# Kernel optimization log

Measured on AMD Instinct MI355X. Metric: run time of the kernel, lower is better.

Reference implementation:

```python
import jax, jax.numpy as jnp
import numpy as np

H = 256; DS = 8; DC = 4; DI = 512; DTR = 16; NH = 4; EPS = 1e-5
B, N, F, E, S, LC = 8, 512, 32, 8192, 512, 8


def setup_inputs() -> dict:
    key = jax.random.key(0)
    ks = iter(jax.random.split(key, 64))
    def rn(shape, s=0.05):
        return jax.random.normal(next(ks), shape, jnp.float32) * s
    z = lambda *s: jnp.zeros(s, jnp.float32)
    inp = dict(
        node_features=jax.random.normal(next(ks), (B, N, F), jnp.float32),
        edge_index=jax.random.randint(next(ks), (B, 2, E), 0, N),
        W_init=rn((F, H)), b_init=z(H),
        gcn1_W=rn((H, H)), gcn1_b=z(H),
        gcn2_W=rn((H, H)), gcn2_b=z(H),
        in_proj_W=rn((H, 2 * DI)),
        conv_W=rn((DI, DC)), conv_b=z(DI),
        xproj_W=rn((DI, DTR + 2 * DS)),
        dt_W=rn((DTR, DI)), dt_b=z(DI),
        A_log=jnp.log(jnp.tile(jnp.arange(1, DS + 1, dtype=jnp.float32), (DI, 1))),
        Dp=jnp.ones((DI,), jnp.float32),
        out_W=rn((DI, H)),
        Wq=rn((H, H)), bq=z(H), Wk=rn((H, H)), bk=z(H), Wv=rn((H, H)), bv=z(H),
        Wo=rn((H, H)), bo=z(H),
        fus_W=rn((3 * H, H)), fus_b=z(H),
        ln_g=jnp.ones((H,), jnp.float32), ln_b=z(H),
        cw=rn((H, 1)), cb=z(1), hw=rn((H, 4)), hb=z(4), tw=rn((H, 3)), tb=z(3),
        p1w=rn((H, S)), p1b=z(S), p2w=rn((H, S)), p2b=z(S),
        dw=rn((H, S)), db=z(S), sw=rn((H, LC)), sb=z(LC))
    return inp


def gcn(x, src, dst, W, b):
    # PyG GCNConv: self-loops + symmetric deg^{-1/2} normalization, scatter-add.
    n = x.shape[0]
    loops = jnp.arange(n)
    s = jnp.concatenate([src, loops]); d = jnp.concatenate([dst, loops])
    deg = jax.ops.segment_sum(jnp.ones_like(d, x.dtype), d, n)
    dinv = jnp.where(deg > 0, jax.lax.rsqrt(deg), 0.0)
    norm = (dinv[s] * dinv[d])[:, None]
    m = x @ W
    return jax.ops.segment_sum(m[s] * norm, d, n) + b


def mamba(x, in_W, conv_W, conv_b, xproj_W, dt_W, dt_b, A_log, Dp, out_W):
    # mamba_ssm Mamba block, batch=1, seq len L = total nodes.
    L = x.shape[0]
    xz = x @ in_W
    xc, zg = xz[:, :DI], xz[:, DI:]
    xp = jnp.pad(xc, ((DC - 1, 0), (0, 0)))            # causal depthwise conv
    win = xp[jnp.arange(L)[:, None] + jnp.arange(DC)[None, :]]  # [L,K,DI]
    xc = jax.nn.silu(jnp.einsum('lkd,dk->ld', win, conv_W) + conv_b)
    proj = xc @ xproj_W
    dt, Bm, Cm = proj[:, :DTR], proj[:, DTR:DTR + DS], proj[:, DTR + DS:]
    delta = jax.nn.softplus(dt @ dt_W + dt_b)           # [L,DI]
    A = -jnp.exp(A_log)                                 # [DI,DS]
    dA = jnp.exp(delta[:, :, None] * A[None])           # [L,DI,DS]
    dBx = delta[:, :, None] * Bm[:, None, :] * xc[:, :, None]
    def step(h, inp):
        dA_t, dBx_t, C_t = inp
        h = dA_t * h + dBx_t
        return h, (h * C_t[None, :]).sum(-1)
    _, y = jax.lax.scan(step, jnp.zeros((DI, DS), x.dtype), (dA, dBx, Cm))
    y = (y + Dp * xc) * jax.nn.silu(zg)
    return y @ out_W


def mha(x, Wq, bq, Wk, bk, Wv, bv, Wo, bo):
    L = x.shape[0]; hd = H // NH
    q = (x @ Wq + bq).reshape(L, NH, hd)
    k = (x @ Wk + bk).reshape(L, NH, hd)
    v = (x @ Wv + bv).reshape(L, NH, hd)
    s = jnp.einsum('qhd,khd->hqk', q, k) / np.float32(np.sqrt(hd))
    a = jax.nn.softmax(s, axis=-1)
    o = jnp.einsum('hqk,khd->qhd', a, v).reshape(L, H)
    return o @ Wo + bo


def _forward(node_features, edge_index, W_init, b_init, gcn1_W, gcn1_b, gcn2_W, gcn2_b,
             in_proj_W, conv_W, conv_b, xproj_W, dt_W, dt_b, A_log, Dp, out_W,
             Wq, bq, Wk, bk, Wv, bv, Wo, bo, fus_W, fus_b, ln_g, ln_b,
             cw, cb, hw, hb, tw, tb, p1w, p1b, p2w, p2b, dw, db, sw, sb):
    Bsz, Nn, Ff = node_features.shape
    x = node_features.reshape(Bsz * Nn, Ff)
    # offset per-graph edge indices into the flat node space (batching loop)
    ei = (edge_index + (jnp.arange(Bsz) * Nn)[:, None, None]).transpose(1, 0, 2).reshape(2, -1)
    src, dst = ei[0], ei[1]
    h = jax.nn.relu(x @ W_init + b_init)
    h = jax.nn.relu(gcn(h, src, dst, gcn1_W, gcn1_b))
    h = jax.nn.relu(gcn(h, src, dst, gcn2_W, gcn2_b))
    m = mamba(h, in_proj_W, conv_W, conv_b, xproj_W, dt_W, dt_b, A_log, Dp, out_W)
    a = mha(h, Wq, bq, Wk, bk, Wv, bv, Wo, bo)
    fused = jax.nn.relu(jnp.concatenate([h, m, a], -1) @ fus_W + fus_b)
    res = fused + h
    mu = res.mean(-1, keepdims=True)
    var = ((res - mu) ** 2).mean(-1, keepdims=True)
    hf = (res - mu) * jax.lax.rsqrt(var + EPS) * ln_g + ln_b
    batch = jnp.repeat(jnp.arange(Bsz), Nn)
    pooled = jax.ops.segment_sum(hf, batch, Bsz) / jnp.float32(Nn)  # global_mean_pool
    outs = [pooled @ cw + cb, pooled @ hw + hb, pooled @ tw + tb,
            pooled @ p1w + p1b, pooled @ p2w + p2b, pooled @ dw + db,
            pooled @ sw + sb]
    return jnp.concatenate(outs, -1)  # [B, 1+4+3+S+S+S+LC]


def reference(node_features, edge_index, W_init, b_init, gcn1_W, gcn1_b, gcn2_W, gcn2_b,
              in_proj_W, conv_W, conv_b, xproj_W, dt_W, dt_b, A_log, Dp, out_W,
              Wq, bq, Wk, bk, Wv, bv, Wo, bo, fus_W, fus_b, ln_g, ln_b,
              cw, cb, hw, hb, tw, tb, p1w, p1b, p2w, p2b, dw, db, sw, sb):
    return _forward(node_features, edge_index, W_init, b_init, gcn1_W, gcn1_b, gcn2_W, gcn2_b,
                    in_proj_W, conv_W, conv_b, xproj_W, dt_W, dt_b, A_log, Dp, out_W,
                    Wq, bq, Wk, bk, Wv, bv, Wo, bo, fus_W, fus_b, ln_g, ln_b,
                    cw, cb, hw, hb, tw, tb, p1w, p1b, p2w, p2b, dw, db, sw, sb)
```

## Files before the change

kernel.cpp:

```cpp
#include <hip/hip_runtime.h>
#include <hip/hip_bf16.h>
#include <math.h>

typedef __hip_bfloat16 hbf;
typedef short bf16x8 __attribute__((ext_vector_type(8)));
typedef float f32x4 __attribute__((ext_vector_type(4)));

constexpr int NL  = 4096;
constexpr int HH  = 256;
constexpr int NE  = 8192;
constexpr int DIc = 512;
constexpr int DSc = 8;
constexpr int CLc = 16;
constexpr int NOUT = 12416;

constexpr size_t O_MBUF  = 0;
constexpr size_t O_QK    = 1048576;
constexpr size_t O_H2    = 2097152;
constexpr size_t O_CATB  = 3145728;
constexpr size_t O_XZB   = 4718592;
constexpr size_t O_XC    = 6815744;
constexpr size_t O_DELTA = 8912896;
constexpr size_t O_PROJ  = 11010048;
constexpr size_t O_HST   = 11141120;
constexpr size_t O_Y     = 12189696;
constexpr size_t O_POOL  = 13238272;
constexpr size_t O_DINV  = 13240320;
constexpr size_t O_B768  = 13244416;
constexpr size_t O_INT   = 13245184;
constexpr size_t O_WT    = 13327112;
constexpr size_t O_XB    = 13839112;
constexpr size_t O_H0B   = 13904648;
constexpr size_t O_H2B   = 14428936;
constexpr size_t O_XCB   = 14953224;
constexpr size_t O_DTAB  = 16001800;
constexpr size_t O_QKB   = 16067584;
constexpr size_t O_VTB   = 17116160;
constexpr size_t O_PART  = 17640448;
constexpr size_t O_HWT   = 17902592;

constexpr int NW = 12;
__device__ __constant__ int wc_cum[NW+1] = {
    0, 8192, 73728, 139264, 155648, 172032, 303104, 565248,
    630784, 696320, 761856, 827392, 1024000 };
__device__ __constant__ int wc_K [NW] = {32,256,256,512,16,512,256,256,256,256,256,768};
__device__ __constant__ int wc_N [NW] = {256,256,256,32,512,256,1024,256,256,256,256,256};
__device__ __constant__ int wc_Kp[NW] = {32,256,256,512,32,512,256,256,256,256,256,768};
struct WSrc { const float* p[NW]; };
struct HSrc { const float* p[7]; };
struct OPtrs { hbf* p[8]; };

__device__ __constant__ int hw_b[8]  = {0,1,5,8,520,1032,1544,1552};
__device__ __constant__ int hw_nc[7] = {1,4,3,512,512,512,8};

constexpr int PR_W = 1024000;
constexpr int PR_X = PR_W + 131072;
constexpr int PR_B = PR_X + 768;
constexpr int PR_P = PR_B + 262144;
constexpr int PR_I = PR_P + 4096;
constexpr int PR_H = PR_I + 397312;
__global__ __launch_bounds__(256) void prep_k(WSrc ws, hbf* __restrict__ wt,
        const float* __restrict__ x, hbf* __restrict__ xb,
        const float* __restrict__ bq, const float* __restrict__ bk,
        const float* __restrict__ bv,
        float* __restrict__ b768, float* __restrict__ part, int* __restrict__ indeg,
        HSrc hs, float* __restrict__ hwt) {
    int idx = blockIdx.x*256 + threadIdx.x;
    if (idx < PR_W) {
        int lo = 0, hi = NW-1;
        while (lo < hi) { int mid = (lo+hi+1)>>1; if (idx >= wc_cum[mid]) lo = mid; else hi = mid-1; }
        int local = idx - wc_cum[lo];
        int Kp = wc_Kp[lo], K = wc_K[lo], N = wc_N[lo];
        int n = local / Kp, k = local - n*Kp;
        float v = (k < K) ? ws.p[lo][(size_t)k*N + n] : 0.0f;
        wt[idx] = __float2bfloat16(v);
    } else if (idx < PR_X) {
        int i = idx - PR_W;
        xb[i] = __float2bfloat16(x[i]);
    } else if (idx < PR_B) {
        int i = idx - PR_X;
        b768[i] = (i < 256) ? bq[i] : (i < 512 ? bk[i-256] : bv[i-512]);
    } else if (idx < PR_P) {
        part[idx - PR_B] = 0.0f;
    } else if (idx < PR_I) {
        indeg[idx - PR_P] = 0;
    } else if (idx < PR_H) {
        int i = idx - PR_I;
        int j = i >> 8, k = i & 255;
        int seg = 0;
        while (j >= hw_b[seg+1]) seg++;
        int col = j - hw_b[seg], nc = hw_nc[seg];
        hwt[(size_t)j*256 + k] = hs.p[seg][(size_t)k*nc + col];
    }
}

__global__ void count_k(const int* __restrict__ ei, int* __restrict__ indeg) {
    int i = blockIdx.x*256 + threadIdx.x;
    int b = i >> 13, e = i & 8191;
    int dst = ei[b*2*NE + NE + e] + (b << 9);
    atomicAdd(&indeg[dst], 1);
}

__global__ __launch_bounds__(1024) void prefix_k(const int* __restrict__ indeg,
                                                 int* __restrict__ row_start,
                                                 int* __restrict__ cursor,
                                                 float* __restrict__ dinv) {
    __shared__ int part[1024];
    int t = threadIdx.x;
    int v0[4]; int s = 0;
    #pragma unroll
    for (int i = 0; i < 4; i++) {
        int cnt = indeg[t*4 + i];
        v0[i] = s; s += cnt;
        dinv[t*4 + i] = rsqrtf(1.0f + (float)cnt);
    }
    part[t] = s;
    __syncthreads();
    for (int o = 1; o < 1024; o <<= 1) {
        int x = (t >= o) ? part[t-o] : 0;
        __syncthreads();
        part[t] += x;
        __syncthreads();
    }
    int base = (t > 0) ? part[t-1] : 0;
    #pragma unroll
    for (int i = 0; i < 4; i++) {
        int rs = base + v0[i];
        row_start[t*4+i] = rs; cursor[t*4+i] = rs;
    }
    if (t == 1023) row_start[4096] = part[1023];
}

__global__ void scatter_k(const int* __restrict__ ei, int* __restrict__ cursor,
                          int* __restrict__ csr) {
    int i = blockIdx.x*256 + threadIdx.x;
    int b = i >> 13, e = i & 8191;
    int src = ei[b*2*NE + e]       + (b << 9);
    int dst = ei[b*2*NE + NE + e]  + (b << 9);
    int pos = atomicAdd(&cursor[dst], 1);
    csr[pos] = src;
}

template<int MODE>
__global__ __launch_bounds__(256) void gather_k(const float* __restrict__ m,
                        const int* __restrict__ csr, const int* __restrict__ row_start,
                        const float* __restrict__ dinv, const float* __restrict__ bias,
                        float* __restrict__ out, hbf* __restrict__ outb,
                        hbf* __restrict__ catb) {
    int n = blockIdx.x, c = threadIdx.x;
    float dn = dinv[n];
    float acc = m[(size_t)n*HH + c] * dn * dn;
    int e0 = row_start[n], e1 = row_start[n+1];
    for (int e = e0; e < e1; e++) {
        int s = csr[e];
        acc += m[(size_t)s*HH + c] * (dinv[s] * dn);
    }
    float r = fmaxf(acc + bias[c], 0.0f);
    if (MODE) {
        out[(size_t)n*HH + c] = r;
        catb[(size_t)n*768 + c] = __float2bfloat16(r);
    }
    outb[(size_t)n*HH + c] = __float2bfloat16(r);
}

template<int ACT, int OUTM>
__global__ __launch_bounds__(512) void mg_k(const unsigned short* __restrict__ A,
        const unsigned short* __restrict__ Bt, const float* __restrict__ bias,
        void* __restrict__ Cp, int ldc, void* __restrict__ Cp2, void* __restrict__ Cp3,
        const float* __restrict__ resid, int ldr, int M, int K, int N)
{
    __shared__ __align__(16) unsigned short Asm[2][64][40];
    __shared__ __align__(16) unsigned short Bsm[2][64][40];
    int t = threadIdx.x;
    int lane = t & 63, w = t >> 6;
    int wm = w & 3, wn = w >> 2;
    int row0 = blockIdx.x * 64, col0 = blockIdx.y * 64;
    int sr = t >> 3;
    int sk8 = (t & 7) * 8;
    int su = sk8 >> 5, so = sk8 & 31;
    f32x4 acc0 = {}, acc1 = {};
    int fr = lane & 15, fq8 = (lane >> 4) * 8;

    uint4 zz = make_uint4(0u,0u,0u,0u);
    uint4 ra = zz, rb = zz;
    bool bnv = (col0 + sr) < N;
    if (sk8 < K) {
        ra = *(const uint4*)&A[(size_t)(row0+sr)*K + sk8];
        if (bnv) rb = *(const uint4*)&Bt[(size_t)(col0+sr)*K + sk8];
    }

    for (int k0 = 0; k0 < K; k0 += 64) {
        __syncthreads();
        *(uint4*)&Asm[su][sr][so] = ra;
        *(uint4*)&Bsm[su][sr][so] = rb;
        __syncthreads();
        int kn = k0 + 64;
        if (kn < K) {
            ra = rb = zz;
            if (kn + sk8 < K) {
                ra = *(const uint4*)&A[(size_t)(row0+sr)*K + kn + sk8];
                if (bnv) rb = *(const uint4*)&Bt[(size_t)(col0+sr)*K + kn + sk8];
            }
        }
        #pragma unroll
        for (int ks = 0; ks < 2; ks++) {
            bf16x8 a  = *(bf16x8*)&Asm[ks][wm*16 + fr][fq8];
            bf16x8 b0 = *(bf16x8*)&Bsm[ks][wn*32 + fr][fq8];
            bf16x8 b1 = *(bf16x8*)&Bsm[ks][wn*32 + 16 + fr][fq8];
            acc0 = __builtin_amdgcn_mfma_f32_16x16x32_bf16(a, b0, acc0, 0, 0, 0);
            acc1 = __builtin_amdgcn_mfma_f32_16x16x32_bf16(a, b1, acc1, 0, 0, 0);
        }
    }

    int fc = lane & 15, frq = (lane >> 4) * 4;
    if constexpr (OUTM == 4) {
        #pragma unroll
        for (int nt = 0; nt < 2; nt++) {
            int col = col0 + wn*32 + nt*16 + fc;
            if (col >= 32) continue;
            f32x4& av = nt ? acc1 : acc0;
            #pragma unroll
            for (int i = 0; i < 4; i++) {
                int row = row0 + wm*16 + frq + i;
                float v = av[i];
                ((float*)Cp)[(size_t)row*32 + col] = v;
                ((hbf*)Cp2)[(size_t)row*32 + col] = __float2bfloat16((col < 16) ? v : 0.0f);
            }
        }
    } else if constexpr (OUTM == 5) {
        if (col0 < 1024) {
            #pragma unroll
            for (int nt = 0; nt < 2; nt++) {
                int col = col0 + wn*32 + nt*16 + fc;
                f32x4& av = nt ? acc1 : acc0;
                #pragma unroll
                for (int i = 0; i < 4; i++) {
                    int row = row0 + wm*16 + frq + i;
                    ((hbf*)Cp)[(size_t)row*1024 + col] = __float2bfloat16(av[i]);
                }
            }
        } else if (col0 < 1536) {
            #pragma unroll
            for (int nt = 0; nt < 2; nt++) {
                int gcol = col0 + wn*32 + nt*16 + fc;
                int col = gcol - 1024;
                float bvv = bias[col];
                float sc = (col < 256) ? 0.125f : 1.0f;
                f32x4& av = nt ? acc1 : acc0;
                #pragma unroll
                for (int i = 0; i < 4; i++) {
                    int row = row0 + wm*16 + frq + i;
                    ((hbf*)Cp2)[(size_t)row*512 + col] = __float2bfloat16((av[i] + bvv) * sc);
                }
            }
        } else {
            __shared__ __align__(16) unsigned short Ts[64][72];
            #pragma unroll
            for (int nt = 0; nt < 2; nt++) {
                int gcol = col0 + wn*32 + nt*16 + fc;
                float bvv = bias[gcol - 1024];
                f32x4& av = nt ? acc1 : acc0;
                #pragma unroll
                for (int i = 0; i < 4; i++)
                    *(hbf*)&Ts[wn*32 + nt*16 + fc][wm*16 + frq + i] = __float2bfloat16(av[i] + bvv);
            }
            __syncthreads();
            int c = t >> 3, rs = (t & 7) * 8;
            *(uint4*)((hbf*)Cp3 + (size_t)(col0 - 1536 + c)*NL + row0 + rs) = *(uint4*)&Ts[c][rs];
        }
    } else {
        #pragma unroll
        for (int nt = 0; nt < 2; nt++) {
            int col = col0 + wn*32 + nt*16 + fc;
            if (col >= N) continue;
            float bvv = bias ? bias[col] : 0.0f;
            f32x4& av = nt ? acc1 : acc0;
            #pragma unroll
            for (int i = 0; i < 4; i++) {
                int row = row0 + wm*16 + frq + i;
                float v = av[i] + bvv;
                if (ACT == 1) v = fmaxf(v, 0.0f);
                if (ACT == 2) v = (v > 20.0f) ? v : log1pf(expf(v));
                if (resid) v += resid[(size_t)row*ldr + col];
                if (OUTM == 0) ((float*)Cp)[(size_t)row*ldc + col] = v;
                else           ((hbf*)Cp)[(size_t)row*ldc + col] = __float2bfloat16(v);
            }
        }
    }
}

__global__ void conv_k(const hbf* __restrict__ xzb, const float* __restrict__ cW,
                       const float* __restrict__ cb, hbf* __restrict__ xcb) {
    int i = blockIdx.x*256 + threadIdx.x;
    int l = i >> 9, d = i & 511;
    float acc = cb[d];
    #pragma unroll
    for (int k = 0; k < 4; k++) {
        int ls = l - 3 + k;
        if (ls >= 0) acc += __bfloat162float(xzb[(size_t)ls*1024 + d]) * cW[d*4 + k];
    }
    float r = acc / (1.0f + __expf(-acc));
    xcb[i] = __float2bfloat16(r);
}

__global__ __launch_bounds__(256) void scan1_k(const float* __restrict__ delta,
                        const hbf* __restrict__ xc, const float* __restrict__ proj,
                        const float* __restrict__ Alog,
                        float* __restrict__ P, float* __restrict__ Hl)
{
    int c = blockIdx.x >> 1;
    int d = ((blockIdx.x & 1) << 8) + threadIdx.x;
    float Ac[DSc], pr[DSc], h[DSc];
    #pragma unroll
    for (int s2 = 0; s2 < DSc; s2++) { Ac[s2] = -__expf(Alog[d*DSc+s2]); pr[s2]=1.0f; h[s2]=0.0f; }
    int l0 = c * CLc;
    for (int l = l0; l < l0 + CLc; l++) {
        float dl = delta[(size_t)l*DIc + d];
        float dx = dl * __bfloat162float(xc[(size_t)l*DIc + d]);
        const float* pb = proj + l*32 + 16;
        #pragma unroll
        for (int s2 = 0; s2 < DSc; s2++) {
            float a = __expf(dl * Ac[s2]);
            h[s2] = a*h[s2] + dx*pb[s2];
            pr[s2] *= a;
        }
    }
    #pragma unroll
    for (int s2 = 0; s2 < DSc; s2++) {
        P [(size_t)(c*DSc+s2)*DIc + d] = pr[s2];
        Hl[(size_t)(c*DSc+s2)*DIc + d] = h[s2];
    }
}

__global__ __launch_bounds__(256) void scan2t_k(const float* __restrict__ P,
                        const float* __restrict__ Hl, float* __restrict__ Hst) {
    __shared__ float Ps[256][17], Hs[256][17];
    int t = threadIdx.x, sg = blockIdx.x;
    int si = t & 15, cb = t >> 4;
    #pragma unroll
    for (int it = 0; it < 16; it++) {
        int c = it*16 + cb;
        size_t off = (size_t)c*4096 + sg*16 + si;
        Ps[c][si] = P[off];
        Hs[c][si] = Hl[off];
    }
    __syncthreads();
    int si2 = t >> 4, g = t & 15;
    int lane = t & 63;
    float Pg = 1.0f, Hg = 0.0f;
    #pragma unroll
    for (int j = 0; j < 16; j++) {
        int c = g*16 + j;
        float pc = Ps[c][si2], hc = Hs[c][si2];
        Hg = hc + pc*Hg;
        Pg = pc*Pg;
    }
    #pragma unroll
    for (int off = 1; off < 16; off <<= 1) {
        float Pp = __shfl(Pg, lane - off);
        float Hp = __shfl(Hg, lane - off);
        if (g >= off) { Hg = Hg + Pg*Hp; Pg = Pg*Pp; }
    }
    float carry = __shfl(Hg, lane - 1);
    if (g == 0) carry = 0.0f;
    float h = carry;
    #pragma unroll
    for (int j = 0; j < 16; j++) {
        int c = g*16 + j;
        float pc = Ps[c][si2], hc = Hs[c][si2];
        Hs[c][si2] = h;
        h = hc + pc*h;
    }
    __syncthreads();
    #pragma unroll
    for (int it = 0; it < 16; it++) {
        int c = it*16 + cb;
        Hst[(size_t)c*4096 + sg*16 + si] = Hs[c][si];
    }
}

__global__ __launch_bounds__(256) void scan3_k(const float* __restrict__ delta,
                        const hbf* __restrict__ xc, const float* __restrict__ proj,
                        const float* __restrict__ Alog, const float* __restrict__ Hst,
                        const float* __restrict__ Dp, const hbf* __restrict__ xzb,
                        hbf* __restrict__ Y)
{
    int c = blockIdx.x >> 1;
    int d = ((blockIdx.x & 1) << 8) + threadIdx.x;
    float Ac[DSc], h[DSc];
    #pragma unroll
    for (int s2 = 0; s2 < DSc; s2++) {
        Ac[s2] = -__expf(Alog[d*DSc+s2]);
        h[s2]  = Hst[(size_t)(c*DSc+s2)*DIc + d];
    }
    float dpv = Dp[d];
    int l0 = c * CLc;
    for (int l = l0; l < l0 + CLc; l++) {
        float dl = delta[(size_t)l*DIc + d];
        float xv = __bfloat162float(xc[(size_t)l*DIc + d]);
        float dx = dl * xv;
        const float* pb = proj + l*32 + 16;
        float y = 0.0f;
        #pragma unroll
        for (int s2 = 0; s2 < DSc; s2++) {
            float a = __expf(dl * Ac[s2]);
            h[s2] = a*h[s2] + dx*pb[s2];
            y += h[s2] * pb[8+s2];
        }
        float z = __bfloat162float(xzb[(size_t)l*1024 + 512 + d]);
        float sz = z / (1.0f + __expf(-z));
        Y[(size_t)l*DIc + d] = __float2bfloat16((y + dpv*xv) * sz);
    }
}

__global__ __launch_bounds__(512, 8) void attn_part_k(const unsigned short* __restrict__ QK,
                       const unsigned short* __restrict__ Vt,
                       OPtrs op, float* __restrict__ lsum)
{
    __shared__ __align__(16) unsigned short QPs[128][72];
    __shared__ __align__(16) unsigned short Ks[64][72];
    __shared__ __align__(16) unsigned short Vs[64][72];
    int t = threadIdx.x, lane = t & 63, w = t >> 6;
    int h = blockIdx.y, q0 = blockIdx.x * 128, skc = blockIdx.z;
    int fm = lane & 15, fq = lane >> 4;

    {
        int qr = t >> 2, qc = (t & 3) * 16;
        const unsigned short* src = &QK[(size_t)(q0+qr)*512 + h*64 + qc];
        *(uint4*)&QPs[qr][qc]     = *(const uint4*)&src[0];
        *(uint4*)&QPs[qr][qc + 8] = *(const uint4*)&src[8];
    }
    __syncthreads();
    bf16x8 qa[2];
    #pragma unroll
    for (int ks = 0; ks < 2; ks++)
        qa[ks] = *(bf16x8*)&QPs[w*16 + fm][ks*32 + fq*8];

    bf16x8 ones;
    #pragma unroll
    for (int j = 0; j < 8; j++) ones[j] = (short)0x3F80;

    f32x4 o[4] = {};
    f32x4 ol = {};
    int sr = t >> 3, sk = (t & 7) * 8;
    const unsigned short* Kb = QK + 256;
    int kt = skc * 512;
    uint4 ka = *(const uint4*)&Kb[(size_t)(kt+sr)*512 + h*64 + sk];
    uint4 va = *(const uint4*)&Vt[(size_t)(h*64+sr)*NL + kt + sk];

    for (int it = 0; it < 8; it++) {
        __syncthreads();
        *(uint4*)&Ks[sr][sk] = ka;
        *(uint4*)&Vs[sr][sk] = va;
        __syncthreads();
        if (it < 7) {
            int kn = kt + 64;
            ka = *(const uint4*)&Kb[(size_t)(kn+sr)*512 + h*64 + sk];
            va = *(const uint4*)&Vt[(size_t)(h*64+sr)*NL + kn + sk];
        }
        f32x4 s[4] = {};
        #pragma unroll
        for (int ks = 0; ks < 2; ks++) {
            #pragma unroll
            for (int nt = 0; nt < 4; nt++) {
                bf16x8 kb = *(bf16x8*)&Ks[nt*16 + fm][ks*32 + fq*8];
                s[nt] = __builtin_amdgcn_mfma_f32_16x16x32_bf16(qa[ks], kb, s[nt], 0, 0, 0);
            }
        }
        #pragma unroll
        for (int nt = 0; nt < 4; nt++)
            #pragma unroll
            for (int i = 0; i < 4; i++) {
                float p = __expf(s[nt][i] - 4.0f);
                *(hbf*)&QPs[w*16 + fq*4 + i][nt*16 + fm] = __float2bfloat16(p);
            }
        #pragma unroll
        for (int ks = 0; ks < 2; ks++) {
            bf16x8 pa = *(bf16x8*)&QPs[w*16 + fm][ks*32 + fq*8];
            #pragma unroll
            for (int nt = 0; nt < 4; nt++) {
                bf16x8 vb = *(bf16x8*)&Vs[nt*16 + fm][ks*32 + fq*8];
                o[nt] = __builtin_amdgcn_mfma_f32_16x16x32_bf16(pa, vb, o[nt], 0, 0, 0);
            }
            ol = __builtin_amdgcn_mfma_f32_16x16x32_bf16(pa, ones, ol, 0, 0, 0);
        }
        kt += 64;
    }
    hbf* Op = op.p[skc];
    #pragma unroll
    for (int i = 0; i < 4; i++) {
        int row = w*16 + fq*4 + i;
        #pragma unroll
        for (int nt = 0; nt < 4; nt++)
            Op[(size_t)(q0 + row)*HH + h*64 + nt*16 + fm] = __float2bfloat16(o[nt][i]);
    }
    if (fm == 0) {
        #pragma unroll
        for (int i = 0; i < 4; i++)
            lsum[(size_t)(skc*4 + h)*NL + q0 + w*16 + fq*4 + i] = ol[i];
    }
}

__global__ __launch_bounds__(256) void amerge_k(OPtrs op, const float* __restrict__ lsum,
                                                hbf* __restrict__ aob) {
    int row = blockIdx.x, t = threadIdx.x, h = t >> 6;
    float L = 0.0f, s = 0.0f;
    #pragma unroll
    for (int c = 0; c < 8; c++) {
        L += lsum[(size_t)(c*4 + h)*NL + row];
        s += __bfloat162float(op.p[c][(size_t)row*HH + t]);
    }
    aob[(size_t)row*HH + t] = __float2bfloat16(s / L);
}

__global__ __launch_bounds__(256) void ln_k(const float* __restrict__ X,
                    const float* __restrict__ g, const float* __restrict__ b,
                    float* __restrict__ part) {
    __shared__ float red[4];
    int r = blockIdx.x, t = threadIdx.x;
    float v = X[(size_t)r*HH + t];
    float s = v;
    #pragma unroll
    for (int o = 32; o > 0; o >>= 1) s += __shfl_down(s, o);
    if ((t & 63) == 0) red[t >> 6] = s;
    __syncthreads();
    float mean = (red[0]+red[1]+red[2]+red[3]) * (1.0f/256.0f);
    float dfv = v - mean;
    float s2 = dfv*dfv;
    #pragma unroll
    for (int o = 32; o > 0; o >>= 1) s2 += __shfl_down(s2, o);
    __syncthreads();
    if ((t & 63) == 0) red[t >> 6] = s2;
    __syncthreads();
    float var = (red[0]+red[1]+red[2]+red[3]) * (1.0f/256.0f);
    float y = dfv * rsqrtf(var + 1e-5f) * g[t] + b[t];
    atomicAdd(&part[(size_t)(r & 127)*2048 + (r >> 9)*HH + t], y * (1.0f/512.0f));
}

__global__ void reduce_k(const float* __restrict__ part, float* __restrict__ pooled) {
    int i = blockIdx.x*256 + threadIdx.x;
    float s = 0.0f;
    #pragma unroll 8
    for (int p = 0; p < 128; p++) s += part[(size_t)p*2048 + i];
    pooled[i] = s;
}

__global__ __launch_bounds__(256) void heads_k(const float* __restrict__ pooled,
        const float* __restrict__ hwt,
        const float* cbh, const float* hb, const float* tb, const float* p1b,
        const float* p2b, const float* db, const float* sb, float* __restrict__ out)
{
    int idx = blockIdx.x*4 + (threadIdx.x >> 6);
    int lane = threadIdx.x & 63;
    if (idx >= NOUT) return;
    int b = idx / 1552, j = idx - b*1552;
    const float* bi; int col;
    if (j < 1)         { bi = cbh; col = j;        }
    else if (j < 5)    { bi = hb;  col = j - 1;    }
    else if (j < 8)    { bi = tb;  col = j - 5;    }
    else if (j < 520)  { bi = p1b; col = j - 8;    }
    else if (j < 1032) { bi = p2b; col = j - 520;  }
    else if (j < 1544) { bi = db;  col = j - 1032; }
    else               { bi = sb;  col = j - 1544; }
    const float* pl = pooled + b*HH;
    const float* wr = hwt + (size_t)j*256;
    float s = 0.0f;
    #pragma unroll
    for (int k = lane; k < 256; k += 64) s = fmaf(pl[k], wr[k], s);
    #pragma unroll
    for (int o = 32; o > 0; o >>= 1) s += __shfl_down(s, o);
    if (lane == 0) out[idx] = s + bi[col];
}

extern "C" void kernel_launch(void* const* d_in, const int* in_sizes, int n_in,
                              void* d_out, int out_size, void* d_ws, size_t ws_size,
                              hipStream_t stream)
{
    (void)in_sizes; (void)n_in; (void)out_size; (void)ws_size;
    const float* x      = (const float*)d_in[0];
    const int*   ei     = (const int*)  d_in[1];
    const float* W_init = (const float*)d_in[2];
    const float* b_init = (const float*)d_in[3];
    const float* g1W = (const float*)d_in[4];
    const float* g1b = (const float*)d_in[5];
    const float* g2W = (const float*)d_in[6];
    const float* g2b = (const float*)d_in[7];
    const float* inW = (const float*)d_in[8];
    const float* cW  = (const float*)d_in[9];
    const float* cb  = (const float*)d_in[10];
    const float* xpW = (const float*)d_in[11];
    const float* dtW = (const float*)d_in[12];
    const float* dtb = (const float*)d_in[13];
    const float* Alog= (const float*)d_in[14];
    const float* Dp  = (const float*)d_in[15];
    const float* outW= (const float*)d_in[16];
    const float* Wq  = (const float*)d_in[17];
    const float* bq  = (const float*)d_in[18];
    const float* Wk  = (const float*)d_in[19];
    const float* bk  = (const float*)d_in[20];
    const float* Wv  = (const float*)d_in[21];
    const float* bv  = (const float*)d_in[22];
    const float* Wo  = (const float*)d_in[23];
    const float* bo  = (const float*)d_in[24];
    const float* fusW= (const float*)d_in[25];
    const float* fusb= (const float*)d_in[26];
    const float* lng = (const float*)d_in[27];
    const float* lnb = (const float*)d_in[28];
    const float* cwp = (const float*)d_in[29];
    const float* cbp = (const float*)d_in[30];
    const float* hwp = (const float*)d_in[31];
    const float* hbp = (const float*)d_in[32];
    const float* twp = (const float*)d_in[33];
    const float* tbp = (const float*)d_in[34];
    const float* p1w = (const float*)d_in[35];
    const float* p1b = (const float*)d_in[36];
    const float* p2w = (const float*)d_in[37];
    const float* p2b = (const float*)d_in[38];
    const float* dwp = (const float*)d_in[39];
    const float* dbp = (const float*)d_in[40];
    const float* swp = (const float*)d_in[41];
    const float* sbp = (const float*)d_in[42];

    float* fw = (float*)d_ws;
    int* iw = (int*)(fw + O_INT);
    int* indeg = iw;
    int* row_start = iw + 4096;
    int* cursor = iw + 8193;
    int* csr = iw + 12289;
    float* dinv = fw + O_DINV;

    hbf* wt   = (hbf*)(fw + O_WT);
    hbf* xb   = (hbf*)(fw + O_XB);
    hbf* h0b  = (hbf*)(fw + O_H0B);
    hbf* h2b  = (hbf*)(fw + O_H2B);
    hbf* xcb  = (hbf*)(fw + O_XCB);
    hbf* dtab = (hbf*)(fw + O_DTAB);
    hbf* xzb  = (hbf*)(fw + O_XZB);
    hbf* yb   = (hbf*)(fw + O_Y);
    hbf* aob  = (hbf*)(fw + O_Y);
    hbf* catb = (hbf*)(fw + O_CATB);
    hbf* qkB  = (hbf*)(fw + O_QKB);
    hbf* vtB  = (hbf*)(fw + O_VTB);
    float* fused = fw + O_XC;
    float* b768 = fw + O_B768;
    float* part = fw + O_PART;
    float* hwt  = fw + O_HWT;

    float* scanP  = fw + O_MBUF;
    float* scanHl = fw + O_QK;
    float* scanHst= fw + O_HST;
    float* lsum   = fw + O_HST;

    OPtrs op;
    op.p[0] = (hbf*)(fw + O_MBUF);
    op.p[1] = (hbf*)(fw + O_MBUF + 524288);
    op.p[2] = (hbf*)(fw + O_DELTA);
    op.p[3] = (hbf*)(fw + O_DELTA + 524288);
    op.p[4] = (hbf*)(fw + O_DELTA + 1048576);
    op.p[5] = (hbf*)(fw + O_DELTA + 1572864);
    op.p[6] = (hbf*)(fw + O_XZB);
    op.p[7] = (hbf*)(fw + O_XZB + 524288);

    hbf* WtInit  = wt + 0;
    hbf* WtG1    = wt + 8192;
    hbf* WtG2    = wt + 73728;
    hbf* WtXp    = wt + 139264;
    hbf* WtDt    = wt + 155648;
    hbf* WtOut   = wt + 172032;
    hbf* WtInQKV = wt + 303104;
    hbf* WtO     = wt + 761856;
    hbf* WtFus   = wt + 827392;

    WSrc wsrc;
    wsrc.p[0]=W_init; wsrc.p[1]=g1W; wsrc.p[2]=g2W; wsrc.p[3]=xpW; wsrc.p[4]=dtW;
    wsrc.p[5]=outW; wsrc.p[6]=inW; wsrc.p[7]=Wq; wsrc.p[8]=Wk; wsrc.p[9]=Wv;
    wsrc.p[10]=Wo; wsrc.p[11]=fusW;
    HSrc hsrc;
    hsrc.p[0]=cwp; hsrc.p[1]=hwp; hsrc.p[2]=twp; hsrc.p[3]=p1w;
    hsrc.p[4]=p2w; hsrc.p[5]=dwp; hsrc.p[6]=swp;
    prep_k<<<(PR_H+255)/256,256,0,stream>>>(wsrc, wt, x, xb, bq, bk, bv, b768,
                                            part, indeg, hsrc, hwt);

    count_k<<<256,256,0,stream>>>(ei, indeg);
    prefix_k<<<1,1024,0,stream>>>(indeg, row_start, cursor, dinv);
    scatter_k<<<256,256,0,stream>>>(ei, cursor, csr);

    mg_k<1,1><<<dim3(64,4),512,0,stream>>>((const unsigned short*)xb, (const unsigned short*)WtInit,
        b_init, h0b, 256, nullptr, nullptr, nullptr, 0, NL, 32, 256);
    mg_k<0,0><<<dim3(64,4),512,0,stream>>>((const unsigned short*)h0b, (const unsigned short*)WtG1,
        nullptr, fw+O_MBUF, 256, nullptr, nullptr, nullptr, 0, NL, 256, 256);
    gather_k<0><<<4096,256,0,stream>>>(fw+O_MBUF, csr, row_start, dinv, g1b, nullptr, h0b, nullptr);
    mg_k<0,0><<<dim3(64,4),512,0,stream>>>((const unsigned short*)h0b, (const unsigned short*)WtG2,
        nullptr, fw+O_MBUF, 256, nullptr, nullptr, nullptr, 0, NL, 256, 256);
    gather_k<1><<<4096,256,0,stream>>>(fw+O_MBUF, csr, row_start, dinv, g2b, fw+O_H2, h2b, catb);

    mg_k<0,5><<<dim3(64,28),512,0,stream>>>((const unsigned short*)h2b, (const unsigned short*)WtInQKV,
        b768, xzb, 1024, qkB, vtB, nullptr, 0, NL, 256, 1792);

    conv_k<<<8192,256,0,stream>>>(xzb, cW, cb, xcb);
    mg_k<0,4><<<dim3(64,1),512,0,stream>>>((const unsigned short*)xcb, (const unsigned short*)WtXp,
        nullptr, fw+O_PROJ, 32, dtab, nullptr, nullptr, 0, NL, 512, 32);
    mg_k<2,0><<<dim3(64,8),512,0,stream>>>((const unsigned short*)dtab, (const unsigned short*)WtDt,
        dtb, fw+O_DELTA, 512, nullptr, nullptr, nullptr, 0, NL, 32, 512);
    scan1_k<<<512,256,0,stream>>>(fw+O_DELTA, xcb, fw+O_PROJ, Alog, scanP, scanHl);
    scan2t_k<<<256,256,0,stream>>>(scanP, scanHl, scanHst);
    scan3_k<<<512,256,0,stream>>>(fw+O_DELTA, xcb, fw+O_PROJ, Alog, scanHst, Dp, xzb, yb);
    mg_k<0,1><<<dim3(64,4),512,0,stream>>>((const unsigned short*)yb, (const unsigned short*)WtOut,
        nullptr, catb + 256, 768, nullptr, nullptr, nullptr, 0, NL, 512, 256);

    attn_part_k<<<dim3(32,4,8),512,0,stream>>>((const unsigned short*)qkB,
        (const unsigned short*)vtB, op, lsum);
    amerge_k<<<4096,256,0,stream>>>(op, lsum, aob);
    mg_k<0,1><<<dim3(64,4),512,0,stream>>>((const unsigned short*)aob, (const unsigned short*)WtO,
        bo, catb + 512, 768, nullptr, nullptr, nullptr, 0, NL, 256, 256);

    mg_k<1,0><<<dim3(64,4),512,0,stream>>>((const unsigned short*)catb, (const unsigned short*)WtFus,
        fusb, fused, 256, nullptr, nullptr, fw+O_H2, 256, NL, 768, 256);
    ln_k<<<4096,256,0,stream>>>(fused, lng, lnb, part);
    reduce_k<<<8,256,0,stream>>>(part, fw+O_POOL);
    heads_k<<<(NOUT+3)/4,256,0,stream>>>(fw+O_POOL, hwt, cbp,hbp,tbp,p1b,p2b,dbp,sbp,
                                         (float*)d_out);
}
```

Measured before the change: 353.8 us.

## Fuse attention merge into Wo GEMM and LayerNorm into fusion GEMM

Adds a wide-tile GEMM kernel (16 rows by 256 cols per block) with two variants. The first folds the split-K attention merge into the A-operand load of the Wo projection. The second applies bias, ReLU, the residual and LayerNorm, then pools with atomics, all in the fusion GEMM epilogue. This drops the amerge_k and ln_k launches and the intermediate aob and fused buffers. The attention score loop is also restructured to compute two tiles at a time, which lowers register pressure. In exchange, LayerNorm variance is now computed as E[x^2]-mu^2, and each block runs only 256 blocks with 16-row tiles.

```diff
diff --git a/kernel.cpp b/kernel.cpp
--- a/kernel.cpp
+++ b/kernel.cpp
@@ -289,6 +289,149 @@
     }
 }
 
+__device__ __forceinline__ uint4 merge_load(const OPtrs& op, const float* __restrict__ lsum,
+                                            int row, int d0) {
+    int head = d0 >> 6;
+    float L = 0.0f;
+    #pragma unroll
+    for (int c = 0; c < 8; c++) L += lsum[(size_t)(c*4 + head)*NL + row];
+    float inv = 1.0f / L;
+    float sums[8] = {};
+    #pragma unroll
+    for (int c = 0; c < 8; c++) {
+        uint4 ov = *(const uint4*)&((const unsigned short*)op.p[c])[(size_t)row*HH + d0];
+        const hbf* oh = (const hbf*)&ov;
+        #pragma unroll
+        for (int j = 0; j < 8; j++) sums[j] += __bfloat162float(oh[j]);
+    }
+    uint4 av;
+    hbf* ah = (hbf*)&av;
+    #pragma unroll
+    for (int j = 0; j < 8; j++) ah[j] = __float2bfloat16(sums[j] * inv);
+    return av;
+}
+
+template<int W>
+__global__ __launch_bounds__(512) void mgw_k(const unsigned short* __restrict__ A,
+        const unsigned short* __restrict__ Bt, const float* __restrict__ bias,
+        hbf* __restrict__ Cb, OPtrs op, const float* __restrict__ lsum,
+        const float* __restrict__ resid, const float* __restrict__ g,
+        const float* __restrict__ bb, float* __restrict__ part, int K)
+{
+    constexpr int KT = (W == 0) ? 4 : 12;
+    __shared__ __align__(16) unsigned short As[2][16][40];
+    __shared__ __align__(16) unsigned short Bs[2][256][40];
+    __shared__ float redS[16][8], redQ[16][8], mval[16], rstd[16];
+    int t = threadIdx.x, lane = t & 63, w = t >> 6;
+    int row0 = blockIdx.x * 16;
+    int fr = lane & 15, fq8 = (lane >> 4) * 8;
+    int sr = t >> 3, sk8 = (t & 7) * 8;
+    f32x4 acc0 = {}, acc1 = {};
+
+    uint4 rb[4]; uint4 ra;
+    #pragma unroll
+    for (int ii = 0; ii < 4; ii++) {
+        int idx = t + ii*512;
+        rb[ii] = *(const uint4*)&Bt[(size_t)(idx >> 3)*K + ((idx & 7) * 8)];
+    }
+    if (t < 128) {
+        if constexpr (W == 0) ra = merge_load(op, lsum, row0 + sr, sk8);
+        else                  ra = *(const uint4*)&A[(size_t)(row0 + sr)*768 + sk8];
+    }
+
+    for (int kt = 0; kt < KT; kt++) {
+        __syncthreads();
+        #pragma unroll
+        for (int ii = 0; ii < 4; ii++) {
+            int idx = t + ii*512;
+            int k8 = (idx & 7) * 8;
+            *(uint4*)&Bs[k8 >> 5][idx >> 3][k8 & 31] = rb[ii];
+        }
+        if (t < 128) *(uint4*)&As[sk8 >> 5][sr][sk8 & 31] = ra;
+        __syncthreads();
+        if (kt + 1 < KT) {
+            int kn = (kt + 1) * 64;
+            #pragma unroll
+            for (int ii = 0; ii < 4; ii++) {
+                int idx = t + ii*512;
+                rb[ii] = *(const uint4*)&Bt[(size_t)(idx >> 3)*K + kn + ((idx & 7) * 8)];
+            }
+            if (t < 128) {
+                if constexpr (W == 0) ra = merge_load(op, lsum, row0 + sr, kn + sk8);
+                else                  ra = *(const uint4*)&A[(size_t)(row0 + sr)*768 + kn + sk8];
+            }
+        }
+        #pragma unroll
+        for (int ks = 0; ks < 2; ks++) {
+            bf16x8 a  = *(bf16x8*)&As[ks][fr][fq8];
+            bf16x8 b0 = *(bf16x8*)&Bs[ks][w*32 + fr][fq8];
+            bf16x8 b1 = *(bf16x8*)&Bs[ks][w*32 + 16 + fr][fq8];
+            acc0 = __builtin_amdgcn_mfma_f32_16x16x32_bf16(a, b0, acc0, 0, 0, 0);
+            acc1 = __builtin_amdgcn_mfma_f32_16x16x32_bf16(a, b1, acc1, 0, 0, 0);
+        }
+    }
+
+    int fc = lane & 15, frq = (lane >> 4) * 4;
+    if constexpr (W == 0) {
+        #pragma unroll
+        for (int nt = 0; nt < 2; nt++) {
+            int col = w*32 + nt*16 + fc;
+            float bvv = bias[col];
+            f32x4& av = nt ? acc1 : acc0;
+            #pragma unroll
+            for (int i = 0; i < 4; i++) {
+                int row = row0 + frq + i;
+                Cb[(size_t)row*768 + col] = __float2bfloat16(av[i] + bvv);
+            }
+        }
+    } else {
+        float v[2][4];
+        #pragma unroll
+        for (int nt = 0; nt < 2; nt++) {
+            int col = w*32 + nt*16 + fc;
+            float bvv = bias[col];
+            f32x4& av = nt ? acc1 : acc0;
+            #pragma unroll
+            for (int i = 0; i < 4; i++) {
+                int row = row0 + frq + i;
+                v[nt][i] = fmaxf(av[i] + bvv, 0.0f) + resid[(size_t)row*HH + col];
+            }
+        }
+        #pragma unroll
+        for (int i = 0; i < 4; i++) {
+            float s = v[0][i] + v[1][i];
+            float q = v[0][i]*v[0][i] + v[1][i]*v[1][i];
+            #pragma unroll
+            for (int o = 1; o < 16; o <<= 1) {
+                s += __shfl_xor(s, o);
+                q += __shfl_xor(q, o);
+            }
+            if (fc == 0) { redS[frq + i][w] = s; redQ[frq + i][w] = q; }
+        }
+        __syncthreads();
+        if (t < 16) {
+            float s = 0.0f, q = 0.0f;
+            #pragma unroll
+            for (int j = 0; j < 8; j++) { s += redS[t][j]; q += redQ[t][j]; }
+            float mu = s * (1.0f/256.0f);
+            float var = q * (1.0f/256.0f) - mu*mu;
+            mval[t] = mu; rstd[t] = rsqrtf(var + 1e-5f);
+        }
+        __syncthreads();
+        #pragma unroll
+        for (int nt = 0; nt < 2; nt++) {
+            int col = w*32 + nt*16 + fc;
+            float gv = g[col], bv2 = bb[col];
+            #pragma unroll
+            for (int i = 0; i < 4; i++) {
+                int r = frq + i, row = row0 + r;
+                float y = (v[nt][i] - mval[r]) * rstd[r] * gv + bv2;
+                atomicAdd(&part[(size_t)(row & 127)*2048 + (row >> 9)*HH + col], y * (1.0f/512.0f));
+            }
+        }
+    }
+}
+
 __global__ void conv_k(const hbf* __restrict__ xzb, const float* __restrict__ cW,
                        const float* __restrict__ cb, hbf* __restrict__ xcb) {
     int i = blockIdx.x*256 + threadIdx.x;
@@ -458,22 +601,24 @@
             ka = *(const uint4*)&Kb[(size_t)(kn+sr)*512 + h*64 + sk];
             va = *(const uint4*)&Vt[(size_t)(h*64+sr)*NL + kn + sk];
         }
-        f32x4 s[4] = {};
-        #pragma unroll
-        for (int ks = 0; ks < 2; ks++) {
-            #pragma unroll
-            for (int nt = 0; nt < 4; nt++) {
-                bf16x8 kb = *(bf16x8*)&Ks[nt*16 + fm][ks*32 + fq*8];
-                s[nt] = __builtin_amdgcn_mfma_f32_16x16x32_bf16(qa[ks], kb, s[nt], 0, 0, 0);
-            }
-        }
-        #pragma unroll
-        for (int nt = 0; nt < 4; nt++)
+        #pragma unroll
+        for (int np = 0; np < 2; np++) {
+            f32x4 s0 = {}, s1 = {};
+            #pragma unroll
+            for (int ks = 0; ks < 2; ks++) {
+                bf16x8 kb0 = *(bf16x8*)&Ks[(np*2+0)*16 + fm][ks*32 + fq*8];
+                bf16x8 kb1 = *(bf16x8*)&Ks[(np*2+1)*16 + fm][ks*32 + fq*8];
+                s0 = __builtin_amdgcn_mfma_f32_16x16x32_bf16(qa[ks], kb0, s0, 0, 0, 0);
+                s1 = __builtin_amdgcn_mfma_f32_16x16x32_bf16(qa[ks], kb1, s1, 0, 0, 0);
+            }
             #pragma unroll
             for (int i = 0; i < 4; i++) {
-                float p = __expf(s[nt][i] - 4.0f);
-                *(hbf*)&QPs[w*16 + fq*4 + i][nt*16 + fm] = __float2bfloat16(p);
-            }
+                float p0 = __expf(s0[i] - 4.0f);
+                float p1 = __expf(s1[i] - 4.0f);
+                *(hbf*)&QPs[w*16 + fq*4 + i][(np*2+0)*16 + fm] = __float2bfloat16(p0);
+                *(hbf*)&QPs[w*16 + fq*4 + i][(np*2+1)*16 + fm] = __float2bfloat16(p1);
+            }
+        }
         #pragma unroll
         for (int ks = 0; ks < 2; ks++) {
             bf16x8 pa = *(bf16x8*)&QPs[w*16 + fm][ks*32 + fq*8];
@@ -499,42 +644,6 @@
         for (int i = 0; i < 4; i++)
             lsum[(size_t)(skc*4 + h)*NL + q0 + w*16 + fq*4 + i] = ol[i];
     }
-}
-
-__global__ __launch_bounds__(256) void amerge_k(OPtrs op, const float* __restrict__ lsum,
-                                                hbf* __restrict__ aob) {
-    int row = blockIdx.x, t = threadIdx.x, h = t >> 6;
-    float L = 0.0f, s = 0.0f;
-    #pragma unroll
-    for (int c = 0; c < 8; c++) {
-        L += lsum[(size_t)(c*4 + h)*NL + row];
-        s += __bfloat162float(op.p[c][(size_t)row*HH + t]);
-    }
-    aob[(size_t)row*HH + t] = __float2bfloat16(s / L);
-}
-
-__global__ __launch_bounds__(256) void ln_k(const float* __restrict__ X,
-                    const float* __restrict__ g, const float* __restrict__ b,
-                    float* __restrict__ part) {
-    __shared__ float red[4];
-    int r = blockIdx.x, t = threadIdx.x;
-    float v = X[(size_t)r*HH + t];
-    float s = v;
-    #pragma unroll
-    for (int o = 32; o > 0; o >>= 1) s += __shfl_down(s, o);
-    if ((t & 63) == 0) red[t >> 6] = s;
-    __syncthreads();
-    float mean = (red[0]+red[1]+red[2]+red[3]) * (1.0f/256.0f);
-    float dfv = v - mean;
-    float s2 = dfv*dfv;
-    #pragma unroll
-    for (int o = 32; o > 0; o >>= 1) s2 += __shfl_down(s2, o);
-    __syncthreads();
-    if ((t & 63) == 0) red[t >> 6] = s2;
-    __syncthreads();
-    float var = (red[0]+red[1]+red[2]+red[3]) * (1.0f/256.0f);
-    float y = dfv * rsqrtf(var + 1e-5f) * g[t] + b[t];
-    atomicAdd(&part[(size_t)(r & 127)*2048 + (r >> 9)*HH + t], y * (1.0f/512.0f));
 }
 
 __global__ void reduce_k(const float* __restrict__ part, float* __restrict__ pooled) {
@@ -637,11 +746,9 @@
     hbf* dtab = (hbf*)(fw + O_DTAB);
     hbf* xzb  = (hbf*)(fw + O_XZB);
     hbf* yb   = (hbf*)(fw + O_Y);
-    hbf* aob  = (hbf*)(fw + O_Y);
     hbf* catb = (hbf*)(fw + O_CATB);
     hbf* qkB  = (hbf*)(fw + O_QKB);
     hbf* vtB  = (hbf*)(fw + O_VTB);
-    float* fused = fw + O_XC;
     float* b768 = fw + O_B768;
     float* part = fw + O_PART;
     float* hwt  = fw + O_HWT;
@@ -710,13 +817,12 @@
 
     attn_part_k<<<dim3(32,4,8),512,0,stream>>>((const unsigned short*)qkB,
         (const unsigned short*)vtB, op, lsum);
-    amerge_k<<<4096,256,0,stream>>>(op, lsum, aob);
-    mg_k<0,1><<<dim3(64,4),512,0,stream>>>((const unsigned short*)aob, (const unsigned short*)WtO,
-        bo, catb + 512, 768, nullptr, nullptr, nullptr, 0, NL, 256, 256);
-
-    mg_k<1,0><<<dim3(64,4),512,0,stream>>>((const unsigned short*)catb, (const unsigned short*)WtFus,
-        fusb, fused, 256, nullptr, nullptr, fw+O_H2, 256, NL, 768, 256);
-    ln_k<<<4096,256,0,stream>>>(fused, lng, lnb, part);
+    mgw_k<0><<<256,512,0,stream>>>(nullptr, (const unsigned short*)WtO, bo,
+        catb + 512, op, lsum, nullptr, nullptr, nullptr, nullptr, 256);
+
+    mgw_k<1><<<256,512,0,stream>>>((const unsigned short*)catb, (const unsigned short*)WtFus,
+        fusb, nullptr, op, nullptr, fw+O_H2, lng, lnb, part, 768);
+
     reduce_k<<<8,256,0,stream>>>(part, fw+O_POOL);
     heads_k<<<(NOUT+3)/4,256,0,stream>>>(fw+O_POOL, hwt, cbp,hbp,tbp,p1b,p2b,dbp,sbp,
                                          (float*)d_out);
```

Measured after the change: 376.8 us. 6.5% more time.

## Aggregate before transform in GCN layers and add MFMA priority hints in attention

Applied to the files above, without the earlier changes.

GCN layers now reorder A·(X·W) into (A·X)·W. The neighbour gather reads bf16 activations instead of fp32 matmul outputs, and bias plus ReLU move into the GEMM epilogue. A new OUTM=6 epilogue writes the fp32, bf16 and concat-buffer copies of the second layer in one pass. The attention kernel splits its QK^T and softmax-exp loop into pairs of tiles and wraps the MFMA sections in s_setprio so math can overlap with exp work from other waves. The gather now accumulates from bf16 inputs and its aggregate is rounded to bf16 before the GEMM, which adds a small precision change.

```diff
diff --git a/kernel.cpp b/kernel.cpp
--- a/kernel.cpp
+++ b/kernel.cpp
@@ -141,26 +141,18 @@
     csr[pos] = src;
 }
 
-template<int MODE>
-__global__ __launch_bounds__(256) void gather_k(const float* __restrict__ m,
+__global__ __launch_bounds__(256) void gather_k(const hbf* __restrict__ m,
                         const int* __restrict__ csr, const int* __restrict__ row_start,
-                        const float* __restrict__ dinv, const float* __restrict__ bias,
-                        float* __restrict__ out, hbf* __restrict__ outb,
-                        hbf* __restrict__ catb) {
+                        const float* __restrict__ dinv, hbf* __restrict__ outb) {
     int n = blockIdx.x, c = threadIdx.x;
     float dn = dinv[n];
-    float acc = m[(size_t)n*HH + c] * dn * dn;
+    float acc = __bfloat162float(m[(size_t)n*HH + c]) * dn * dn;
     int e0 = row_start[n], e1 = row_start[n+1];
     for (int e = e0; e < e1; e++) {
         int s = csr[e];
-        acc += m[(size_t)s*HH + c] * (dinv[s] * dn);
-    }
-    float r = fmaxf(acc + bias[c], 0.0f);
-    if (MODE) {
-        out[(size_t)n*HH + c] = r;
-        catb[(size_t)n*768 + c] = __float2bfloat16(r);
-    }
-    outb[(size_t)n*HH + c] = __float2bfloat16(r);
+        acc += __bfloat162float(m[(size_t)s*HH + c]) * (dinv[s] * dn);
+    }
+    outb[(size_t)n*HH + c] = __float2bfloat16(acc);
 }
 
 template<int ACT, int OUTM>
@@ -268,6 +260,22 @@
             int c = t >> 3, rs = (t & 7) * 8;
             *(uint4*)((hbf*)Cp3 + (size_t)(col0 - 1536 + c)*NL + row0 + rs) = *(uint4*)&Ts[c][rs];
         }
+    } else if constexpr (OUTM == 6) {
+        #pragma unroll
+        for (int nt = 0; nt < 2; nt++) {
+            int col = col0 + wn*32 + nt*16 + fc;
+            float bvv = bias[col];
+            f32x4& av = nt ? acc1 : acc0;
+            #pragma unroll
+            for (int i = 0; i < 4; i++) {
+                int row = row0 + wm*16 + frq + i;
+                float v = fmaxf(av[i] + bvv, 0.0f);
+                ((float*)Cp)[(size_t)row*HH + col] = v;
+                hbf hv = __float2bfloat16(v);
+                ((hbf*)Cp2)[(size_t)row*HH + col] = hv;
+                ((hbf*)Cp3)[(size_t)row*768 + col] = hv;
+            }
+        }
     } else {
         #pragma unroll
         for (int nt = 0; nt < 2; nt++) {
@@ -458,22 +466,27 @@
             ka = *(const uint4*)&Kb[(size_t)(kn+sr)*512 + h*64 + sk];
             va = *(const uint4*)&Vt[(size_t)(h*64+sr)*NL + kn + sk];
         }
-        f32x4 s[4] = {};
-        #pragma unroll
-        for (int ks = 0; ks < 2; ks++) {
-            #pragma unroll
-            for (int nt = 0; nt < 4; nt++) {
-                bf16x8 kb = *(bf16x8*)&Ks[nt*16 + fm][ks*32 + fq*8];
-                s[nt] = __builtin_amdgcn_mfma_f32_16x16x32_bf16(qa[ks], kb, s[nt], 0, 0, 0);
-            }
-        }
-        #pragma unroll
-        for (int nt = 0; nt < 4; nt++)
+        #pragma unroll
+        for (int np = 0; np < 2; np++) {
+            f32x4 s0 = {}, s1 = {};
+            __builtin_amdgcn_s_setprio(1);
+            #pragma unroll
+            for (int ks = 0; ks < 2; ks++) {
+                bf16x8 kb0 = *(bf16x8*)&Ks[(np*2+0)*16 + fm][ks*32 + fq*8];
+                bf16x8 kb1 = *(bf16x8*)&Ks[(np*2+1)*16 + fm][ks*32 + fq*8];
+                s0 = __builtin_amdgcn_mfma_f32_16x16x32_bf16(qa[ks], kb0, s0, 0, 0, 0);
+                s1 = __builtin_amdgcn_mfma_f32_16x16x32_bf16(qa[ks], kb1, s1, 0, 0, 0);
+            }
+            __builtin_amdgcn_s_setprio(0);
             #pragma unroll
             for (int i = 0; i < 4; i++) {
-                float p = __expf(s[nt][i] - 4.0f);
-                *(hbf*)&QPs[w*16 + fq*4 + i][nt*16 + fm] = __float2bfloat16(p);
-            }
+                float p0 = __expf(s0[i] - 4.0f);
+                float p1 = __expf(s1[i] - 4.0f);
+                *(hbf*)&QPs[w*16 + fq*4 + i][(np*2+0)*16 + fm] = __float2bfloat16(p0);
+                *(hbf*)&QPs[w*16 + fq*4 + i][(np*2+1)*16 + fm] = __float2bfloat16(p1);
+            }
+        }
+        __builtin_amdgcn_s_setprio(1);
         #pragma unroll
         for (int ks = 0; ks < 2; ks++) {
             bf16x8 pa = *(bf16x8*)&QPs[w*16 + fm][ks*32 + fq*8];
@@ -484,6 +497,7 @@
             }
             ol = __builtin_amdgcn_mfma_f32_16x16x32_bf16(pa, ones, ol, 0, 0, 0);
         }
+        __builtin_amdgcn_s_setprio(0);
         kt += 64;
     }
     hbf* Op = op.p[skc];
@@ -641,6 +655,7 @@
     hbf* catb = (hbf*)(fw + O_CATB);
     hbf* qkB  = (hbf*)(fw + O_QKB);
     hbf* vtB  = (hbf*)(fw + O_VTB);
+    hbf* aggb = (hbf*)(fw + O_MBUF);
     float* fused = fw + O_XC;
     float* b768 = fw + O_B768;
     float* part = fw + O_PART;
@@ -687,12 +702,12 @@
 
     mg_k<1,1><<<dim3(64,4),512,0,stream>>>((const unsigned short*)xb, (const unsigned short*)WtInit,
         b_init, h0b, 256, nullptr, nullptr, nullptr, 0, NL, 32, 256);
-    mg_k<0,0><<<dim3(64,4),512,0,stream>>>((const unsigned short*)h0b, (const unsigned short*)WtG1,
-        nullptr, fw+O_MBUF, 256, nullptr, nullptr, nullptr, 0, NL, 256, 256);
-    gather_k<0><<<4096,256,0,stream>>>(fw+O_MBUF, csr, row_start, dinv, g1b, nullptr, h0b, nullptr);
-    mg_k<0,0><<<dim3(64,4),512,0,stream>>>((const unsigned short*)h0b, (const unsigned short*)WtG2,
-        nullptr, fw+O_MBUF, 256, nullptr, nullptr, nullptr, 0, NL, 256, 256);
-    gather_k<1><<<4096,256,0,stream>>>(fw+O_MBUF, csr, row_start, dinv, g2b, fw+O_H2, h2b, catb);
+    gather_k<<<4096,256,0,stream>>>(h0b, csr, row_start, dinv, aggb);
+    mg_k<1,1><<<dim3(64,4),512,0,stream>>>((const unsigned short*)aggb, (const unsigned short*)WtG1,
+        g1b, h0b, 256, nullptr, nullptr, nullptr, 0, NL, 256, 256);
+    gather_k<<<4096,256,0,stream>>>(h0b, csr, row_start, dinv, aggb);
+    mg_k<1,6><<<dim3(64,4),512,0,stream>>>((const unsigned short*)aggb, (const unsigned short*)WtG2,
+        g2b, fw+O_H2, 256, h2b, catb, nullptr, 0, NL, 256, 256);
 
     mg_k<0,5><<<dim3(64,28),512,0,stream>>>((const unsigned short*)h2b, (const unsigned short*)WtInQKV,
         b768, xzb, 1024, qkB, vtB, nullptr, 0, NL, 256, 1792);
```

Result: no change. 354.9 us (+0.3%).
